# Optimization experiments

Measured on AMD Instinct MI355X. Metric: run time of the kernel, lower is better.

## Reference

```python
import jax, jax.numpy as jnp
import numpy as np

N_FEATURES = 256
RAND_RANGE = 100.0


def _random_embed(x):
    """Deterministic pseudo-random embedding: each scalar in x seeds a counter-based
    RNG producing N_FEATURES uniforms in [0, RAND_RANGE). (JAX threefry replaces
    Python's Mersenne Twister; same structure: value-seeded deterministic uniforms.)"""
    flat = jax.lax.stop_gradient(x).reshape(-1)
    seeds = jax.lax.bitcast_convert_type(flat, jnp.uint32)  # value -> integer seed
    base = jax.random.key(42)
    keys = jax.vmap(lambda s: jax.random.fold_in(base, s))(seeds)
    emb = jax.vmap(lambda k: jax.random.uniform(k, (N_FEATURES,), minval=0.0, maxval=RAND_RANGE))(keys)
    return emb.reshape(x.shape + (N_FEATURES,))  # [B, S, F]


def setup_inputs() -> dict:
    key = jax.random.key(0)
    kx, kw, kb = jax.random.split(key, 3)
    x = jax.random.normal(kx, (256, 512), dtype=jnp.float32)
    W = jax.random.normal(kw, (N_FEATURES, N_FEATURES), dtype=jnp.float32) * 0.05
    b = jax.random.normal(kb, (N_FEATURES,), dtype=jnp.float32) * 0.05
    return {"x": x, "W": W, "b": b}


def reference(x, W, b):
    emb = _random_embed(x)                      # [B, S, F]
    out = jnp.einsum('bsf,gf->bsg', emb, W) + b  # nn.Linear: emb @ W.T + b
    return out
```

## Files before the change

kernel.cpp:

```cpp
#include <hip/hip_runtime.h>
#include <stdint.h>

#define F 256
#define R 64
#define THREADS 256
#define GCH 32
#define NCH (F / GCH)
#define CH_SLOTS (GCH * F / 8)

typedef __attribute__((ext_vector_type(8))) short short8;
typedef __attribute__((ext_vector_type(4))) float floatx4;

__device__ __forceinline__ uint32_t rotl32(uint32_t x, int d) {
  return (x << d) | (x >> (32 - d));
}

__device__ __forceinline__ void tf2x32(uint32_t k0, uint32_t k1,
                                       uint32_t x0, uint32_t x1,
                                       uint32_t& o0, uint32_t& o1) {
  const uint32_t k2 = k0 ^ k1 ^ 0x1BD11BDAu;
  x0 += k0; x1 += k1;
#define TF_R4(a,b,c,d)                                    \
  x0 += x1; x1 = rotl32(x1,(a)); x1 ^= x0;                \
  x0 += x1; x1 = rotl32(x1,(b)); x1 ^= x0;                \
  x0 += x1; x1 = rotl32(x1,(c)); x1 ^= x0;                \
  x0 += x1; x1 = rotl32(x1,(d)); x1 ^= x0;
  TF_R4(13,15,26,6)
  x0 += k1; x1 += k2 + 1u;
  TF_R4(17,29,16,24)
  x0 += k2; x1 += k0 + 2u;
  TF_R4(13,15,26,6)
  x0 += k0; x1 += k1 + 3u;
  TF_R4(17,29,16,24)
  x0 += k1; x1 += k2 + 4u;
  TF_R4(13,15,26,6)
  x0 += k2; x1 += k0 + 5u;
#undef TF_R4
  o0 = x0; o1 = x1;
}

__device__ __forceinline__ uint32_t f2bf(float f) {
  uint32_t u = __float_as_uint(f);
  u += 0x7FFFu + ((u >> 16) & 1u);
  return u >> 16;
}

__device__ __forceinline__ uint32_t feat_bf16(uint32_t k0, uint32_t k1, uint32_t i) {
  uint32_t o0, o1;
  tf2x32(k0, k1, 0u, i, o0, o1);
  return f2bf((float)(o0 ^ o1) * 2.3283064365386963e-8f);
}

__device__ __forceinline__ void gl_lds16(const void* gptr, void* lptr) {
  __builtin_amdgcn_global_load_lds(
      (const __attribute__((address_space(1))) uint32_t*)gptr,
      (__attribute__((address_space(3))) uint32_t*)lptr, 16, 0, 0);
}

__global__ __launch_bounds__(256) void femb_conv(const float* __restrict__ W,
                                                 uint16_t* __restrict__ ws) {
  int s = blockIdx.x * 256 + threadIdx.x;
  int gt = s >> 10;
  int c = (s >> 5) & 31;
  int g = s & 31;
  const float4* src = (const float4*)(W + (size_t)(gt * GCH + g) * F + c * 8);
  float4 v0 = src[0], v1 = src[1];
  short8 o;
  o[0] = (short)f2bf(v0.x); o[1] = (short)f2bf(v0.y);
  o[2] = (short)f2bf(v0.z); o[3] = (short)f2bf(v0.w);
  o[4] = (short)f2bf(v1.x); o[5] = (short)f2bf(v1.y);
  o[6] = (short)f2bf(v1.z); o[7] = (short)f2bf(v1.w);
  *(short8*)(ws + (size_t)s * 8) = o;
}

__global__ __launch_bounds__(THREADS, 4) void femb_main(
    const float* __restrict__ x, const uint16_t* __restrict__ Wbf,
    const float* __restrict__ bias, float* __restrict__ out) {
  __shared__ uint16_t sW[2][GCH * F];

  const int tid  = threadIdx.x;
  const int lane = tid & 63;
  const int wave = tid >> 6;
  const int qd   = lane >> 4;
  const int l16  = lane & 15;
  const size_t row0 = (size_t)blockIdx.x * R;
  const int myrow = (int)row0 + wave * 16 + l16;

  float xv = x[myrow];

  {
    const uint16_t* src = Wbf;
    #pragma unroll
    for (int it = 0; it < CH_SLOTS / THREADS; ++it) {
      int sbase = it * THREADS + wave * 64;
      gl_lds16(src + (size_t)(sbase + lane) * 8, &sW[0][(size_t)sbase * 8]);
    }
  }

  uint32_t k0, k1;
  tf2x32(0u, 42u, 0u, __float_as_uint(xv), k0, k1);

  short8 afrag[8];
  #pragma unroll
  for (int kt = 0; kt < 8; ++kt) {
    const uint32_t fb = (uint32_t)(kt * 32 + qd * 8);
    uint32_t w32[4];
    #pragma unroll
    for (int p = 0; p < 4; ++p) {
      uint32_t lo = feat_bf16(k0, k1, fb + 2 * p);
      uint32_t hi = feat_bf16(k0, k1, fb + 2 * p + 1);
      w32[p] = lo | (hi << 16);
    }
    union { uint32_t w[4]; short8 s; } u;
    u.w[0] = w32[0]; u.w[1] = w32[1]; u.w[2] = w32[2]; u.w[3] = w32[3];
    afrag[kt] = u.s;
  }

  for (int gt = 0; gt < NCH; ++gt) {
    __syncthreads();
    if (gt + 1 < NCH) {
      const uint16_t* src = Wbf + (size_t)(gt + 1) * CH_SLOTS * 8;
      #pragma unroll
      for (int it = 0; it < CH_SLOTS / THREADS; ++it) {
        int sbase = it * THREADS + wave * 64;
        gl_lds16(src + (size_t)(sbase + lane) * 8,
                 &sW[(gt + 1) & 1][(size_t)sbase * 8]);
      }
    }

    const uint16_t* buf = sW[gt & 1];
    floatx4 acc[2];
    acc[0] = (floatx4){0.f, 0.f, 0.f, 0.f};
    acc[1] = (floatx4){0.f, 0.f, 0.f, 0.f};
    #pragma unroll
    for (int kt = 0; kt < 8; ++kt) {
      int c = kt * 4 + qd;
      #pragma unroll
      for (int n = 0; n < 2; ++n) {
        short8 b = *(const short8*)&buf[(size_t)(c * 32 + n * 16 + l16) * 8];
        acc[n] = __builtin_amdgcn_mfma_f32_16x16x32_bf16(afrag[kt], b, acc[n], 0, 0, 0);
      }
    }

    #pragma unroll
    for (int n = 0; n < 2; ++n) {
      int g = gt * GCH + n * 16 + l16;
      float bg = bias[g];
      #pragma unroll
      for (int reg = 0; reg < 4; ++reg) {
        size_t grow = row0 + (size_t)wave * 16 + qd * 4 + reg;
        out[grow * F + g] = acc[n][reg] + bg;
      }
    }
  }
}

extern "C" void kernel_launch(void* const* d_in, const int* in_sizes, int n_in,
                              void* d_out, int out_size, void* d_ws, size_t ws_size,
                              hipStream_t stream) {
  const float* x = (const float*)d_in[0];
  const float* W = (const float*)d_in[1];
  const float* b = (const float*)d_in[2];
  float* out = (float*)d_out;
  uint16_t* wsbf = (uint16_t*)d_ws;
  const int nrows = in_sizes[0];
  const int blocks = nrows / R;

  hipLaunchKernelGGL(femb_conv, dim3((F * F / 8) / 256), dim3(256), 0, stream, W, wsbf);
  hipLaunchKernelGGL(femb_main, dim3(blocks), dim3(THREADS), 0, stream,
                     x, wsbf, b, out);
}
```

Measured before the change: 189.4 us.

## Drop LDS staging of W, read B fragments from global; interleave threefry pairs

Removes the double-buffered LDS staging of the bf16 weight chunks and the per-chunk block barriers, so each wave loads its MFMA B fragments straight from global memory and relies on L1/L2 reuse. The threefry generator is restructured to precompute key-schedule constants and to compute two counters at once for more ILP. Rotation now uses alignbit and bf16 packing uses a single perm. The risk is higher global/L2 traffic and load latency exposed inside the MFMA loop without explicit prefetching.

```diff
diff --git a/kernel.cpp b/kernel.cpp
--- a/kernel.cpp
+++ b/kernel.cpp
@@ -12,49 +12,63 @@
 typedef __attribute__((ext_vector_type(4))) float floatx4;
 
 __device__ __forceinline__ uint32_t rotl32(uint32_t x, int d) {
-  return (x << d) | (x >> (32 - d));
+  return __builtin_amdgcn_alignbit(x, x, (uint32_t)(32 - d));
 }
 
-__device__ __forceinline__ void tf2x32(uint32_t k0, uint32_t k1,
-                                       uint32_t x0, uint32_t x1,
-                                       uint32_t& o0, uint32_t& o1) {
-  const uint32_t k2 = k0 ^ k1 ^ 0x1BD11BDAu;
-  x0 += k0; x1 += k1;
-#define TF_R4(a,b,c,d)                                    \
-  x0 += x1; x1 = rotl32(x1,(a)); x1 ^= x0;                \
-  x0 += x1; x1 = rotl32(x1,(b)); x1 ^= x0;                \
-  x0 += x1; x1 = rotl32(x1,(c)); x1 ^= x0;                \
-  x0 += x1; x1 = rotl32(x1,(d)); x1 ^= x0;
-  TF_R4(13,15,26,6)
-  x0 += k1; x1 += k2 + 1u;
-  TF_R4(17,29,16,24)
-  x0 += k2; x1 += k0 + 2u;
-  TF_R4(13,15,26,6)
-  x0 += k0; x1 += k1 + 3u;
-  TF_R4(17,29,16,24)
-  x0 += k1; x1 += k2 + 4u;
-  TF_R4(13,15,26,6)
-  x0 += k2; x1 += k0 + 5u;
-#undef TF_R4
-  o0 = x0; o1 = x1;
+struct TFK { uint32_t k0, k1, k2, a1, a2, a3, a4, a5; };
+
+__device__ __forceinline__ TFK mkkeys(uint32_t k0, uint32_t k1) {
+  TFK K;
+  K.k0 = k0; K.k1 = k1; K.k2 = k0 ^ k1 ^ 0x1BD11BDAu;
+  K.a1 = K.k2 + 1u; K.a2 = k0 + 2u; K.a3 = k1 + 3u;
+  K.a4 = K.k2 + 4u; K.a5 = k0 + 5u;
+  return K;
+}
+
+__device__ __forceinline__ void tf_one(const TFK& K, uint32_t& x0, uint32_t& x1) {
+  x0 += K.k0; x1 += K.k1;
+#define TF1(r) x0 += x1; x1 = rotl32(x1, r); x1 ^= x0;
+  TF1(13) TF1(15) TF1(26) TF1(6)   x0 += K.k1; x1 += K.a1;
+  TF1(17) TF1(29) TF1(16) TF1(24)  x0 += K.k2; x1 += K.a2;
+  TF1(13) TF1(15) TF1(26) TF1(6)   x0 += K.k0; x1 += K.a3;
+  TF1(17) TF1(29) TF1(16) TF1(24)  x0 += K.k1; x1 += K.a4;
+  TF1(13) TF1(15) TF1(26) TF1(6)   x0 += K.k2; x1 += K.a5;
+#undef TF1
+}
+
+__device__ __forceinline__ void tf_pair(const TFK& K, uint32_t i,
+                                        uint32_t& oa, uint32_t& ob) {
+  uint32_t a0 = K.k0, a1 = K.k1 + i;
+  uint32_t b0 = K.k0, b1 = K.k1 + i + 1u;
+#define TF2(r)  a0 += a1; b0 += b1;                         \
+                a1 = rotl32(a1, r); b1 = rotl32(b1, r);     \
+                a1 ^= a0; b1 ^= b0;
+#define INJ2(u, v) a0 += (u); b0 += (u); a1 += (v); b1 += (v);
+  TF2(13) TF2(15) TF2(26) TF2(6)   INJ2(K.k1, K.a1)
+  TF2(17) TF2(29) TF2(16) TF2(24)  INJ2(K.k2, K.a2)
+  TF2(13) TF2(15) TF2(26) TF2(6)   INJ2(K.k0, K.a3)
+  TF2(17) TF2(29) TF2(16) TF2(24)  INJ2(K.k1, K.a4)
+  TF2(13) TF2(15) TF2(26) TF2(6)   INJ2(K.k2, K.a5)
+#undef TF2
+#undef INJ2
+  oa = a0 ^ a1;
+  ob = b0 ^ b1;
+}
+
+__device__ __forceinline__ uint32_t featpack(const TFK& K, uint32_t i) {
+  uint32_t xa, xb;
+  tf_pair(K, i, xa, xb);
+  uint32_t ulo = __float_as_uint((float)xa * 2.3283064365386963e-8f);
+  uint32_t uhi = __float_as_uint((float)xb * 2.3283064365386963e-8f);
+  ulo += 0x7FFFu + ((ulo >> 16) & 1u);
+  uhi += 0x7FFFu + ((uhi >> 16) & 1u);
+  return __builtin_amdgcn_perm(uhi, ulo, 0x07060302u);
 }
 
 __device__ __forceinline__ uint32_t f2bf(float f) {
   uint32_t u = __float_as_uint(f);
   u += 0x7FFFu + ((u >> 16) & 1u);
   return u >> 16;
-}
-
-__device__ __forceinline__ uint32_t feat_bf16(uint32_t k0, uint32_t k1, uint32_t i) {
-  uint32_t o0, o1;
-  tf2x32(k0, k1, 0u, i, o0, o1);
-  return f2bf((float)(o0 ^ o1) * 2.3283064365386963e-8f);
-}
-
-__device__ __forceinline__ void gl_lds16(const void* gptr, void* lptr) {
-  __builtin_amdgcn_global_load_lds(
-      (const __attribute__((address_space(1))) uint32_t*)gptr,
-      (__attribute__((address_space(3))) uint32_t*)lptr, 16, 0, 0);
 }
 
 __global__ __launch_bounds__(256) void femb_conv(const float* __restrict__ W,
@@ -76,8 +90,6 @@
 __global__ __launch_bounds__(THREADS, 4) void femb_main(
     const float* __restrict__ x, const uint16_t* __restrict__ Wbf,
     const float* __restrict__ bias, float* __restrict__ out) {
-  __shared__ uint16_t sW[2][GCH * F];
-
   const int tid  = threadIdx.x;
   const int lane = tid & 63;
   const int wave = tid >> 6;
@@ -88,17 +100,10 @@
 
   float xv = x[myrow];
 
-  {
-    const uint16_t* src = Wbf;
-    #pragma unroll
-    for (int it = 0; it < CH_SLOTS / THREADS; ++it) {
-      int sbase = it * THREADS + wave * 64;
-      gl_lds16(src + (size_t)(sbase + lane) * 8, &sW[0][(size_t)sbase * 8]);
-    }
-  }
-
-  uint32_t k0, k1;
-  tf2x32(0u, 42u, 0u, __float_as_uint(xv), k0, k1);
+  TFK K42 = mkkeys(0u, 42u);
+  uint32_t s0 = 0u, s1 = __float_as_uint(xv);
+  tf_one(K42, s0, s1);
+  const TFK K = mkkeys(s0, s1);
 
   short8 afrag[8];
   #pragma unroll
@@ -106,29 +111,16 @@
     const uint32_t fb = (uint32_t)(kt * 32 + qd * 8);
     uint32_t w32[4];
     #pragma unroll
-    for (int p = 0; p < 4; ++p) {
-      uint32_t lo = feat_bf16(k0, k1, fb + 2 * p);
-      uint32_t hi = feat_bf16(k0, k1, fb + 2 * p + 1);
-      w32[p] = lo | (hi << 16);
-    }
+    for (int p = 0; p < 4; ++p)
+      w32[p] = featpack(K, fb + 2 * p);
     union { uint32_t w[4]; short8 s; } u;
     u.w[0] = w32[0]; u.w[1] = w32[1]; u.w[2] = w32[2]; u.w[3] = w32[3];
     afrag[kt] = u.s;
   }
 
+  #pragma unroll 1
   for (int gt = 0; gt < NCH; ++gt) {
-    __syncthreads();
-    if (gt + 1 < NCH) {
-      const uint16_t* src = Wbf + (size_t)(gt + 1) * CH_SLOTS * 8;
-      #pragma unroll
-      for (int it = 0; it < CH_SLOTS / THREADS; ++it) {
-        int sbase = it * THREADS + wave * 64;
-        gl_lds16(src + (size_t)(sbase + lane) * 8,
-                 &sW[(gt + 1) & 1][(size_t)sbase * 8]);
-      }
-    }
-
-    const uint16_t* buf = sW[gt & 1];
+    const uint16_t* Wc = Wbf + (size_t)gt * CH_SLOTS * 8;
     floatx4 acc[2];
     acc[0] = (floatx4){0.f, 0.f, 0.f, 0.f};
     acc[1] = (floatx4){0.f, 0.f, 0.f, 0.f};
@@ -137,7 +129,7 @@
       int c = kt * 4 + qd;
       #pragma unroll
       for (int n = 0; n < 2; ++n) {
-        short8 b = *(const short8*)&buf[(size_t)(c * 32 + n * 16 + l16) * 8];
+        short8 b = *(const short8*)(Wc + (size_t)(c * 32 + n * 16 + l16) * 8);
         acc[n] = __builtin_amdgcn_mfma_f32_16x16x32_bf16(afrag[kt], b, acc[n], 0, 0, 0);
       }
     }
```

Result: slower. 195.1 us (+3.0%).
